# Optimization experiments

Measured on AMD Instinct MI355X. Metric: run time of the kernel, lower is better.

Reference implementation:

```python
import jax, jax.numpy as jnp
import numpy as np

DIM = 1024
NUM_HEADS = 16
HEAD_DIM = DIM // NUM_HEADS
SCALE = HEAD_DIM ** -0.25
EPS = 1e-5


def layer_norm(x, w, b):
    mu = jnp.mean(x, axis=-1, keepdims=True)
    var = jnp.var(x, axis=-1, keepdims=True)
    return (x - mu) * jax.lax.rsqrt(var + EPS) * w + b


def setup_inputs() -> dict:
    key = jax.random.key(0)
    ks = jax.random.split(key, 10)
    b, l, d = 2, 2048, DIM
    x = jax.random.normal(ks[0], (b, l, d), dtype=jnp.float32)
    # causal mask, broadcastable over heads: [b, 1, l, l]
    causal = jnp.tril(jnp.ones((l, l), dtype=jnp.int32))
    mask = jnp.broadcast_to(causal[None, None], (b, 1, l, l))
    s = 0.02
    return {
        "x": x,
        "mask": mask,
        "ln1_w": jnp.ones((d,), jnp.float32),
        "ln1_b": jnp.zeros((d,), jnp.float32),
        "qkv_w": jax.random.normal(ks[1], (d, 3 * d), jnp.float32) * s,
        "qkv_b": jnp.zeros((3 * d,), jnp.float32),
        "proj_w": jax.random.normal(ks[2], (d, d), jnp.float32) * s,
        "proj_b": jnp.zeros((d,), jnp.float32),
        "ln2_w": jnp.ones((d,), jnp.float32),
        "ln2_b": jnp.zeros((d,), jnp.float32),
        "ffn_w1": jax.random.normal(ks[3], (d, 4 * d), jnp.float32) * s,
        "ffn_b1": jnp.zeros((4 * d,), jnp.float32),
        "ffn_w2": jax.random.normal(ks[4], (4 * d, d), jnp.float32) * s,
        "ffn_b2": jnp.zeros((d,), jnp.float32),
    }


def attention(x, mask, qkv_w, qkv_b, proj_w, proj_b):
    b, l, d = x.shape
    n, c = NUM_HEADS, HEAD_DIM
    qkv = (x @ qkv_w + qkv_b).reshape(b, l, n * 3, c)
    q, k, v = qkv[:, :, :n], qkv[:, :, n:2 * n], qkv[:, :, 2 * n:]
    # scores: [b, n, l, l], scale applied to both q and k (head_dim^-0.25 each)
    attn = jnp.einsum('binc,bjnc->bnij', q * SCALE, k * SCALE)
    attn = jnp.where(mask[:, :, :l, :l] == 0, -jnp.inf, attn)
    attn = jax.nn.softmax(attn.astype(jnp.float32), axis=-1).astype(x.dtype)
    out = jnp.einsum('bnij,bjnc->binc', attn, v).reshape(b, l, d)
    return out @ proj_w + proj_b


def reference(x, mask, ln1_w, ln1_b, qkv_w, qkv_b, proj_w, proj_b,
              ln2_w, ln2_b, ffn_w1, ffn_b1, ffn_w2, ffn_b2):
    h = x + attention(layer_norm(x, ln1_w, ln1_b), mask, qkv_w, qkv_b, proj_w, proj_b)
    y = layer_norm(h, ln2_w, ln2_b)
    ffn = jax.nn.gelu(y @ ffn_w1 + ffn_b1, approximate=False) @ ffn_w2 + ffn_b2
    return h + ffn
```

## Files before the change

kernel.cpp:

```cpp
#include <hip/hip_runtime.h>
#include <hip/hip_bf16.h>
#include <math.h>

typedef __attribute__((ext_vector_type(8))) short bf16x8;
typedef __attribute__((ext_vector_type(4))) float f32x4;
typedef __attribute__((ext_vector_type(4))) unsigned u32x4;

#define MFMA16(a, b, c) __builtin_amdgcn_mfma_f32_16x16x32_bf16((a), (b), (c), 0, 0, 0)

typedef const __attribute__((address_space(1))) void* gas_ptr;
typedef __attribute__((address_space(3))) void* las_ptr;

#define QK_SCALE 0.18033688011112042f

__device__ __forceinline__ unsigned pack_bf16(float a, float b) {
    unsigned ua = (unsigned)__bfloat16_as_ushort(__float2bfloat16(a));
    unsigned ub = (unsigned)__bfloat16_as_ushort(__float2bfloat16(b));
    return ua | (ub << 16);
}

__global__ __launch_bounds__(256)
void transpose_all(const float* __restrict__ qkv_w, const float* __restrict__ proj_w,
                   const float* __restrict__ ffn_w1, const float* __restrict__ ffn_w2,
                   __hip_bfloat16* __restrict__ wqkv, __hip_bfloat16* __restrict__ wproj,
                   __hip_bfloat16* __restrict__ wff1, __hip_bfloat16* __restrict__ wff2)
{
    const int bid = blockIdx.x;
    const float* in; __hip_bfloat16* out; int K, N, r;
    if (bid < 3072)      { in = qkv_w;  out = wqkv;  K = 1024; N = 3072; r = bid;        }
    else if (bid < 4096) { in = proj_w; out = wproj; K = 1024; N = 1024; r = bid - 3072; }
    else if (bid < 8192) { in = ffn_w1; out = wff1;  K = 1024; N = 4096; r = bid - 4096; }
    else                 { in = ffn_w2; out = wff2;  K = 4096; N = 1024; r = bid - 8192; }
    const int ncols = N >> 5;
    const int n0 = (r % ncols) * 32, k0 = (r / ncols) * 32;

    __shared__ float t[32][33];
    const int tx = threadIdx.x & 31, ty = threadIdx.x >> 5;
    #pragma unroll
    for (int j = 0; j < 32; j += 8)
        t[ty + j][tx] = in[(size_t)(k0 + ty + j) * N + n0 + tx];
    __syncthreads();
    #pragma unroll
    for (int j = 0; j < 32; j += 8)
        out[(size_t)(n0 + ty + j) * K + k0 + tx] = __float2bfloat16(t[tx][ty + j]);
}

__global__ __launch_bounds__(256)
void ln_kernel(const float* __restrict__ in, const float* __restrict__ w,
               const float* __restrict__ b, __hip_bfloat16* __restrict__ out)
{
    const int row = blockIdx.x;
    const int tid = threadIdx.x;
    const float4 v = reinterpret_cast<const float4*>(in + (size_t)row * 1024)[tid];
    float s  = v.x + v.y + v.z + v.w;
    float s2 = v.x * v.x + v.y * v.y + v.z * v.z + v.w * v.w;
    #pragma unroll
    for (int off = 32; off > 0; off >>= 1) {
        s  += __shfl_down(s,  off);
        s2 += __shfl_down(s2, off);
    }
    __shared__ float red[8];
    const int wv = tid >> 6, ln = tid & 63;
    if (ln == 0) { red[wv] = s; red[4 + wv] = s2; }
    __syncthreads();
    s  = red[0] + red[1] + red[2] + red[3];
    s2 = red[4] + red[5] + red[6] + red[7];
    const float mu   = s * (1.0f / 1024.0f);
    const float var  = s2 * (1.0f / 1024.0f) - mu * mu;
    const float rstd = rsqrtf(var + 1e-5f);
    const float4 wv4 = reinterpret_cast<const float4*>(w)[tid];
    const float4 bv4 = reinterpret_cast<const float4*>(b)[tid];
    const size_t o = (size_t)row * 1024 + tid * 4;
    out[o + 0] = __float2bfloat16((v.x - mu) * rstd * wv4.x + bv4.x);
    out[o + 1] = __float2bfloat16((v.y - mu) * rstd * wv4.y + bv4.y);
    out[o + 2] = __float2bfloat16((v.z - mu) * rstd * wv4.z + bv4.z);
    out[o + 3] = __float2bfloat16((v.w - mu) * rstd * wv4.w + bv4.w);
}

template<int MODE>
__global__ __launch_bounds__(256, 3)
void gemm128p(const __hip_bfloat16* __restrict__ A,
              const __hip_bfloat16* __restrict__ Bt,
              const float* __restrict__ bias,
              void* __restrict__ C0, void* __restrict__ C1,
              int N, int K)
{
    constexpr int SLOT = 8192;
    __shared__ __align__(16) __hip_bfloat16 lds[3 * SLOT];

    const int tid  = threadIdx.x;
    const int lane = tid & 63;
    const int w    = tid >> 6;
    const int wr   = w >> 1, wc = w & 1;
    const int fr   = lane & 15, fq = lane >> 4;

    const int nwg = gridDim.x * gridDim.y;
    int flat = blockIdx.y * gridDim.x + blockIdx.x;
    flat = (flat & 7) * (nwg >> 3) + (flat >> 3);
    const int bx = flat % gridDim.x, by = flat / gridDim.x;
    const int m0 = by * 128, n0 = bx * 128;
    const int NT = K >> 5;

    const int prc = w * 8 + (lane >> 3);
    const int ch  = lane & 7;
    const __hip_bfloat16* aS[2];
    const __hip_bfloat16* bS[2];
    #pragma unroll
    for (int j = 0; j < 2; ++j) {
        const int pr  = prc + 32 * j;
        const int v   = ch ^ (pr & 7);
        const int row = 2 * pr + (v >> 2);
        const int col = 8 * (v & 3);
        aS[j] = A  + (size_t)(m0 + row) * K + col;
        bS[j] = Bt + (size_t)(n0 + row) * K + col;
    }

    auto stage = [&](int kt, int s) {
        __hip_bfloat16* LA = &lds[s * SLOT];
        __hip_bfloat16* LB = LA + 4096;
        #pragma unroll
        for (int j = 0; j < 2; ++j) {
            __builtin_amdgcn_global_load_lds((gas_ptr)(const void*)(aS[j] + kt * 32),
                                             (las_ptr)(void*)(LA + w * 512 + j * 2048), 16, 0, 0);
            __builtin_amdgcn_global_load_lds((gas_ptr)(const void*)(bS[j] + kt * 32),
                                             (las_ptr)(void*)(LB + w * 512 + j * 2048), 16, 0, 0);
        }
    };

    f32x4 acc[4][4] = {};

    stage(0, 0);
    stage(1, 1);
    int sl = 0, sp = 2;

    for (int kt = 0; kt < NT; ++kt) {
        if (kt + 1 < NT)
            asm volatile("s_waitcnt vmcnt(4) lgkmcnt(0)" ::: "memory");
        else
            asm volatile("s_waitcnt vmcnt(0) lgkmcnt(0)" ::: "memory");
        __builtin_amdgcn_s_barrier();
        __builtin_amdgcn_sched_barrier(0);

        if (kt + 2 < NT) stage(kt + 2, sp);

        const __hip_bfloat16* LA = &lds[sl * SLOT];
        const __hip_bfloat16* LB = LA + 4096;
        bf16x8 af[4], bg[4];
        #pragma unroll
        for (int m = 0; m < 4; ++m) {
            const int r = wr * 64 + m * 16 + fr;
            af[m] = *reinterpret_cast<const bf16x8*>(
                &LA[(r >> 1) * 64 + (((r & 1) * 32 + fq * 8) ^ (((r >> 1) & 7) * 8))]);
        }
        #pragma unroll
        for (int n = 0; n < 4; ++n) {
            const int r = wc * 64 + n * 16 + fr;
            bg[n] = *reinterpret_cast<const bf16x8*>(
                &LB[(r >> 1) * 64 + (((r & 1) * 32 + fq * 8) ^ (((r >> 1) & 7) * 8))]);
        }

        __builtin_amdgcn_s_setprio(1);
        #pragma unroll
        for (int m = 0; m < 4; ++m)
            #pragma unroll
            for (int n = 0; n < 4; ++n)
                acc[m][n] = MFMA16(af[m], bg[n], acc[m][n]);
        __builtin_amdgcn_s_setprio(0);

        sl = (sl == 2) ? 0 : sl + 1;
        sp = (sp == 2) ? 0 : sp + 1;
    }

    __syncthreads();
    ushort* E = reinterpret_cast<ushort*>(lds);
    auto eaddr = [](int r, int c16) { return r * 128 + (((c16) ^ ((r >> 3) & 15)) << 3); };

    const float qsc = (MODE == 3 && n0 < 1024) ? QK_SCALE : 1.0f;
    #pragma unroll
    for (int n = 0; n < 4; ++n) {
        const int col = wc * 64 + n * 16 + fr;
        const float bv = bias[n0 + col];
        #pragma unroll
        for (int m = 0; m < 4; ++m) {
            #pragma unroll
            for (int i = 0; i < 4; ++i) {
                const int row = wr * 64 + m * 16 + fq * 4 + i;
                float v = acc[m][n][i] + bv;
                if (MODE == 2) v = 0.5f * v * (1.0f + erff(v * 0.70710678118654752f));
                if (MODE == 3) v *= qsc;
                E[eaddr(row, col >> 3) + (col & 7)] =
                    __bfloat16_as_ushort(__float2bfloat16(v));
            }
        }
    }
    __syncthreads();

    if (MODE == 3 && n0 >= 2048) {
        const int bq    = m0 >> 11;
        const int lbase = m0 & 2047;
        const int hcb   = n0 - 2048;
        #pragma unroll
        for (int p = 0; p < 8; ++p) {
            const int id  = p * 256 + tid;
            const int hcl = id >> 4;
            const int lc  = id & 15;
            u32x4 pkt;
            #pragma unroll
            for (int k2 = 0; k2 < 4; ++k2) {
                const int l0 = lc * 8 + k2 * 2;
                const unsigned a = E[eaddr(l0,     hcl >> 3) + (hcl & 7)];
                const unsigned b = E[eaddr(l0 + 1, hcl >> 3) + (hcl & 7)];
                pkt[k2] = a | (b << 16);
            }
            *reinterpret_cast<u32x4*>(
                &reinterpret_cast<__hip_bfloat16*>(C1)
                    [((size_t)(bq * 1024 + hcb + hcl) << 11) + lbase + lc * 8]) = pkt;
        }
        return;
    }

    const size_t ldC = (MODE == 3) ? 2048 : (size_t)N;
    __hip_bfloat16* Cb = reinterpret_cast<__hip_bfloat16*>(C0);
    #pragma unroll
    for (int p = 0; p < 8; ++p) {
        const int id  = p * 256 + tid;
        const int row = id >> 4;
        const int c16 = id & 15;
        const bf16x8 vv = *reinterpret_cast<const bf16x8*>(&E[eaddr(row, c16)]);
        *reinterpret_cast<bf16x8*>(&Cb[(size_t)(m0 + row) * ldC + n0 + c16 * 8]) = vv;
    }
}

__global__ __launch_bounds__(512, 1)
void gemm256g(const __hip_bfloat16* __restrict__ A,
              const __hip_bfloat16* __restrict__ Bt,
              const float* __restrict__ bias,
              __hip_bfloat16* __restrict__ C0,
              int N, int K)
{
    constexpr int SLOT = 16384;
    __shared__ __align__(16) __hip_bfloat16 lds[4 * SLOT];

    const int tid  = threadIdx.x;
    const int lane = tid & 63;
    const int w    = tid >> 6;
    const int wm   = w >> 2, wn = w & 3;
    const int fr   = lane & 15, fq = lane >> 4;

    const int nwg = gridDim.x * gridDim.y;
    int flat = blockIdx.y * gridDim.x + blockIdx.x;
    flat = (flat & 7) * (nwg >> 3) + (flat >> 3);
    const int bx = flat % gridDim.x, by = flat / gridDim.x;
    const int m0 = by * 256, n0 = bx * 256;
    const int NT = K >> 5;

    const __hip_bfloat16* aS[2];
    const __hip_bfloat16* bS[2];
    #pragma unroll
    for (int j = 0; j < 2; ++j) {
        const int c   = tid + 512 * j;
        const int row = c >> 2;
        const int lc  = (c & 3) ^ ((row >> 1) & 3);
        aS[j] = A  + (size_t)(m0 + row) * K + lc * 8;
        bS[j] = Bt + (size_t)(n0 + row) * K + lc * 8;
    }

    auto stageA = [&](int kt) {
        __hip_bfloat16* L = &lds[(kt & 3) * SLOT];
        #pragma unroll
        for (int j = 0; j < 2; ++j)
            __builtin_amdgcn_global_load_lds((gas_ptr)(const void*)(aS[j] + kt * 32),
                                             (las_ptr)(void*)(L + w * 512 + j * 4096), 16, 0, 0);
    };
    auto stageB = [&](int kt) {
        __hip_bfloat16* L = &lds[(kt & 3) * SLOT] + 8192;
        #pragma unroll
        for (int j = 0; j < 2; ++j)
            __builtin_amdgcn_global_load_lds((gas_ptr)(const void*)(bS[j] + kt * 32),
                                             (las_ptr)(void*)(L + w * 512 + j * 4096), 16, 0, 0);
    };

    f32x4 acc[8][4] = {};

    stageA(0); stageB(0);
    stageA(1); stageB(1);
    stageA(2); stageB(2);
    asm volatile("s_waitcnt vmcnt(8)" ::: "memory");
    __builtin_amdgcn_s_barrier();
    __builtin_amdgcn_sched_barrier(0);

    for (int kt = 0; kt < NT; ++kt) {
        const __hip_bfloat16* LA = &lds[(kt & 3) * SLOT];
        const __hip_bfloat16* LB = LA + 8192;
        bf16x8 af[4], bg[4];

        #pragma unroll
        for (int m = 0; m < 4; ++m) {
            const int r = wm * 128 + m * 16 + fr;
            af[m] = *reinterpret_cast<const bf16x8*>(
                &LA[r * 32 + ((fq ^ ((r >> 1) & 3)) << 3)]);
        }
        #pragma unroll
        for (int n = 0; n < 4; ++n) {
            const int r = wn * 64 + n * 16 + fr;
            bg[n] = *reinterpret_cast<const bf16x8*>(
                &LB[r * 32 + ((fq ^ ((r >> 1) & 3)) << 3)]);
        }
        if (kt + 3 < NT) stageA(kt + 3);
        __builtin_amdgcn_sched_barrier(0);
        __builtin_amdgcn_s_barrier();
        asm volatile("s_waitcnt lgkmcnt(0)" ::: "memory");
        __builtin_amdgcn_sched_barrier(0);
        __builtin_amdgcn_s_setprio(1);
        #pragma unroll
        for (int m = 0; m < 4; ++m)
            #pragma unroll
            for (int n = 0; n < 4; ++n)
                acc[m][n] = MFMA16(af[m], bg[n], acc[m][n]);
        __builtin_amdgcn_s_setprio(0);
        __builtin_amdgcn_sched_barrier(0);
        __builtin_amdgcn_s_barrier();

        #pragma unroll
        for (int m = 0; m < 4; ++m) {
            const int r = wm * 128 + 64 + m * 16 + fr;
            af[m] = *reinterpret_cast<const bf16x8*>(
                &LA[r * 32 + ((fq ^ ((r >> 1) & 3)) << 3)]);
        }
        if (kt + 3 < NT) stageB(kt + 3);
        __builtin_amdgcn_sched_barrier(0);
        __builtin_amdgcn_s_barrier();
        asm volatile("s_waitcnt lgkmcnt(0)" ::: "memory");
        __builtin_amdgcn_sched_barrier(0);
        __builtin_amdgcn_s_setprio(1);
        #pragma unroll
        for (int m = 0; m < 4; ++m)
            #pragma unroll
            for (int n = 0; n < 4; ++n)
                acc[4 + m][n] = MFMA16(af[m], bg[n], acc[4 + m][n]);
        __builtin_amdgcn_s_setprio(0);
        __builtin_amdgcn_sched_barrier(0);
        if (kt + 3 < NT)      asm volatile("s_waitcnt vmcnt(8)" ::: "memory");
        else if (kt + 2 < NT) asm volatile("s_waitcnt vmcnt(4)" ::: "memory");
        else                  asm volatile("s_waitcnt vmcnt(0)" ::: "memory");
        __builtin_amdgcn_s_barrier();
    }

    __syncthreads();
    ushort* E = reinterpret_cast<ushort*>(lds);
    auto eaddr = [](int r, int c16) { return r * 256 + (((c16) ^ (r & 31)) << 3); };

    #pragma unroll
    for (int n = 0; n < 4; ++n) {
        const int col = wn * 64 + n * 16 + fr;
        const float bv = bias[n0 + col];
        #pragma unroll
        for (int a = 0; a < 8; ++a) {
            #pragma unroll
            for (int i = 0; i < 4; ++i) {
                const int row = wm * 128 + (a >> 2) * 64 + (a & 3) * 16 + fq * 4 + i;
                float v = acc[a][n][i] + bv;
                v = 0.5f * v * (1.0f + erff(v * 0.70710678118654752f));
                E[eaddr(row, col >> 3) + (col & 7)] =
                    __bfloat16_as_ushort(__float2bfloat16(v));
            }
        }
    }
    __syncthreads();

    #pragma unroll
    for (int p = 0; p < 16; ++p) {
        const int id  = p * 512 + tid;
        const int row = id >> 5;
        const int c16 = id & 31;
        const bf16x8 vv = *reinterpret_cast<const bf16x8*>(&E[eaddr(row, c16)]);
        *reinterpret_cast<bf16x8*>(&C0[(size_t)(m0 + row) * N + n0 + c16 * 8]) = vv;
    }
}

__global__ __launch_bounds__(256, 3)
void gemm_n64(const __hip_bfloat16* __restrict__ A,
              const __hip_bfloat16* __restrict__ Bt,
              const float* __restrict__ bias,
              const float* __restrict__ resid,
              float* __restrict__ C0,
              int N, int K)
{
    constexpr int SLOT = 6144;
    __shared__ __align__(16) __hip_bfloat16 lds[3 * SLOT];

    const int tid  = threadIdx.x;
    const int lane = tid & 63;
    const int w    = tid >> 6;
    const int wr   = w >> 1, wc = w & 1;
    const int fr   = lane & 15, fq = lane >> 4;

    const int nwg = gridDim.x * gridDim.y;
    int flat = blockIdx.y * gridDim.x + blockIdx.x;
    flat = (flat & 7) * (nwg >> 3) + (flat >> 3);
    const int bx = flat % gridDim.x, by = flat / gridDim.x;
    const int m0 = by * 128, n0 = bx * 64;
    const int NT = K >> 5;

    const int prc = w * 8 + (lane >> 3);
    const int ch  = lane & 7;
    const __hip_bfloat16* aS[2];
    #pragma unroll
    for (int j = 0; j < 2; ++j) {
        const int pr  = prc + 32 * j;
        const int v   = ch ^ (pr & 7);
        aS[j] = A + (size_t)(m0 + 2 * pr + (v >> 2)) * K + 8 * (v & 3);
    }
    const __hip_bfloat16* bS;
    {
        const int c  = w * 64 + lane;
        const int pr = c >> 3;
        const int v  = (c & 7) ^ (pr & 7);
        bS = Bt + (size_t)(n0 + 2 * pr + (v >> 2)) * K + 8 * (v & 3);
    }

    auto stage = [&](int kt, int s) {
        __hip_bfloat16* LA = &lds[s * SLOT];
        __hip_bfloat16* LB = LA + 4096;
        #pragma unroll
        for (int j = 0; j < 2; ++j)
            __builtin_amdgcn_global_load_lds((gas_ptr)(const void*)(aS[j] + kt * 32),
                                             (las_ptr)(void*)(LA + w * 512 + j * 2048), 16, 0, 0);
        __builtin_amdgcn_global_load_lds((gas_ptr)(const void*)(bS + kt * 32),
                                         (las_ptr)(void*)(LB + w * 512), 16, 0, 0);
    };

    f32x4 acc[4][2] = {};

    stage(0, 0);
    stage(1, 1);
    int sl = 0, sp = 2;

    for (int kt = 0; kt < NT; ++kt) {
        if (kt + 1 < NT)
            asm volatile("s_waitcnt vmcnt(3) lgkmcnt(0)" ::: "memory");
        else
            asm volatile("s_waitcnt vmcnt(0) lgkmcnt(0)" ::: "memory");
        __builtin_amdgcn_s_barrier();
        __builtin_amdgcn_sched_barrier(0);

        if (kt + 2 < NT) stage(kt + 2, sp);

        const __hip_bfloat16* LA = &lds[sl * SLOT];
        const __hip_bfloat16* LB = LA + 4096;
        bf16x8 af[4], bg[2];
        #pragma unroll
        for (int m = 0; m < 4; ++m) {
            const int r = wr * 64 + m * 16 + fr;
            af[m] = *reinterpret_cast<const bf16x8*>(
                &LA[(r >> 1) * 64 + (((r & 1) * 32 + fq * 8) ^ (((r >> 1) & 7) * 8))]);
        }
        #pragma unroll
        for (int n = 0; n < 2; ++n) {
            const int r = wc * 32 + n * 16 + fr;
            bg[n] = *reinterpret_cast<const bf16x8*>(
                &LB[(r >> 1) * 64 + (((r & 1) * 32 + fq * 8) ^ (((r >> 1) & 7) * 8))]);
        }

        __builtin_amdgcn_s_setprio(1);
        #pragma unroll
        for (int m = 0; m < 4; ++m)
            #pragma unroll
            for (int n = 0; n < 2; ++n)
                acc[m][n] = MFMA16(af[m], bg[n], acc[m][n]);
        __builtin_amdgcn_s_setprio(0);

        sl = (sl == 2) ? 0 : sl + 1;
        sp = (sp == 2) ? 0 : sp + 1;
    }

    #pragma unroll
    for (int n = 0; n < 2; ++n) {
        const int col = n0 + wc * 32 + n * 16 + fr;
        const float bv = bias[col];
        #pragma unroll
        for (int m = 0; m < 4; ++m)
            #pragma unroll
            for (int i = 0; i < 4; ++i) {
                const int row = m0 + wr * 64 + m * 16 + fq * 4 + i;
                C0[(size_t)row * N + col] = acc[m][n][i] + bv + resid[(size_t)row * N + col];
            }
    }
}

__global__ __launch_bounds__(256)
void attn_kernel(const __hip_bfloat16* __restrict__ qk,
                 const __hip_bfloat16* __restrict__ Vt,
                 __hip_bfloat16* __restrict__ out)
{
    const int bid  = blockIdx.x;
    const int xcd  = bid & 7;
    const int rank = bid >> 3;
    const int panel = xcd * 4 + (rank & 3);
    const int qt   = 31 - (rank >> 2);
    const int h = panel & 15, b = panel >> 4;
    const int q0 = qt * 64;

    const int lane = threadIdx.x & 63;
    const int w    = threadIdx.x >> 6;
    const int fr   = lane & 15, fq = lane >> 4;
    const int qrow = q0 + w * 16 + fr;

    __shared__ __align__(16) __hip_bfloat16 Klds[2][64 * 64];
    __shared__ __align__(16) __hip_bfloat16 Vlds[2][64 * 64];

    bf16x8 qf[2];
    {
        const __hip_bfloat16* qp = qk + ((size_t)(b * 2048 + qrow) << 11) + h * 64 + fq * 8;
        qf[0] = *reinterpret_cast<const bf16x8*>(qp);
        qf[1] = *reinterpret_cast<const bf16x8*>(qp + 32);
    }

    const int srow8 = lane >> 3;
    const int sc    = lane & 7;
    const __hip_bfloat16* Kg[2];
    const __hip_bfloat16* Vg[2];
    #pragma unroll
    for (int j = 0; j < 2; ++j) {
        const int r = w * 16 + j * 8 + srow8;
        const int csw = (sc ^ (r & 7)) * 8;
        Kg[j] = qk + ((size_t)(b * 2048 + r) << 11) + 1024 + h * 64 + csw;
        Vg[j] = Vt + ((size_t)(b * 1024 + h * 64 + r) << 11) + csw;
    }

    auto stage = [&](int kv0, int bufi) {
        __hip_bfloat16* KL = &Klds[bufi][0];
        __hip_bfloat16* VL = &Vlds[bufi][0];
        #pragma unroll
        for (int j = 0; j < 2; ++j) {
            __builtin_amdgcn_global_load_lds(
                (gas_ptr)(const void*)(Kg[j] + ((size_t)kv0 << 11)),
                (las_ptr)(void*)&KL[(w * 16 + j * 8) * 64], 16, 0, 0);
            __builtin_amdgcn_global_load_lds(
                (gas_ptr)(const void*)(Vg[j] + kv0),
                (las_ptr)(void*)&VL[(w * 16 + j * 8) * 64], 16, 0, 0);
        }
    };

    float m_run = -1e30f, l_run = 0.0f;
    f32x4 o[4] = {};

    const int ntiles = qt + 1;
    stage(0, 0);
    int cur = 0;

    for (int t = 0; t < ntiles; ++t) {
        const int kv0 = t << 6;
        __syncthreads();
        if (t + 1 < ntiles) stage((t + 1) << 6, cur ^ 1);

        const __hip_bfloat16* Kl = &Klds[cur][0];
        const __hip_bfloat16* Vl = &Vlds[cur][0];

        f32x4 s[4] = {};
        #pragma unroll
        for (int n = 0; n < 4; ++n) {
            const int row = n * 16 + fr;
            const int sw = (row & 7) << 3;
            const bf16x8 k0 = *reinterpret_cast<const bf16x8*>(&Kl[row * 64 + ((fq * 8) ^ sw)]);
            const bf16x8 k1 = *reinterpret_cast<const bf16x8*>(&Kl[row * 64 + ((fq * 8 + 32) ^ sw)]);
            s[n] = MFMA16(k0, qf[0], s[n]);
            s[n] = MFMA16(k1, qf[1], s[n]);
        }

        float pm = -1e30f;
        if (t == ntiles - 1) {
            #pragma unroll
            for (int n = 0; n < 4; ++n)
                #pragma unroll
                for (int i = 0; i < 4; ++i) {
                    const int kvp = kv0 + n * 16 + fq * 4 + i;
                    float sv = s[n][i];
                    sv = (kvp <= qrow) ? sv : -1e30f;
                    s[n][i] = sv;
                    pm = fmaxf(pm, sv);
                }
        } else {
            #pragma unroll
            for (int n = 0; n < 4; ++n)
                #pragma unroll
                for (int i = 0; i < 4; ++i)
                    pm = fmaxf(pm, s[n][i]);
        }
        pm = fmaxf(pm, __shfl_xor(pm, 16));
        pm = fmaxf(pm, __shfl_xor(pm, 32));

        if (!__all(pm <= m_run + 8.0f)) {
            const float mnew = fmaxf(m_run, pm);
            const float corr = exp2f(m_run - mnew);
            m_run = mnew;
            l_run *= corr;
            #pragma unroll
            for (int i = 0; i < 4; ++i) {
                const float ci = __shfl(corr, fq * 4 + i);
                o[0][i] *= ci; o[1][i] *= ci; o[2][i] *= ci; o[3][i] *= ci;
            }
        }

        float rs = 0.0f;
        unsigned pk[8];
        #pragma unroll
        for (int n = 0; n < 4; ++n) {
            const float p0 = exp2f(s[n][0] - m_run);
            const float p1 = exp2f(s[n][1] - m_run);
            const float p2 = exp2f(s[n][2] - m_run);
            const float p3 = exp2f(s[n][3] - m_run);
            rs += (p0 + p1) + (p2 + p3);
            pk[n * 2 + 0] = pack_bf16(p0, p1);
            pk[n * 2 + 1] = pack_bf16(p2, p3);
        }
        rs += __shfl_xor(rs, 16);
        rs += __shfl_xor(rs, 32);
        l_run += rs;

        u32x4 A0, A1;
        #pragma unroll
        for (int r = 0; r < 4; ++r) {
            const int slx = fr + ((2 * (fq & 1) + (r >> 1)) << 4);
            const unsigned lo0 = __shfl(pk[0 + (r & 1)], slx);
            const unsigned hi0 = __shfl(pk[2 + (r & 1)], slx);
            const unsigned lo1 = __shfl(pk[4 + (r & 1)], slx);
            const unsigned hi1 = __shfl(pk[6 + (r & 1)], slx);
            A0[r] = (fq & 2) ? hi0 : lo0;
            A1[r] = (fq & 2) ? hi1 : lo1;
        }
        const bf16x8 pa0 = __builtin_bit_cast(bf16x8, A0);
        const bf16x8 pa1 = __builtin_bit_cast(bf16x8, A1);

        #pragma unroll
        for (int tt = 0; tt < 4; ++tt) {
            const int row = tt * 16 + fr;
            const int sw = (row & 7) << 3;
            const bf16x8 v0 = *reinterpret_cast<const bf16x8*>(&Vl[row * 64 + ((fq * 8) ^ sw)]);
            const bf16x8 v1 = *reinterpret_cast<const bf16x8*>(&Vl[row * 64 + ((fq * 8 + 32) ^ sw)]);
            o[tt] = MFMA16(pa0, v0, o[tt]);
            o[tt] = MFMA16(pa1, v1, o[tt]);
        }
        cur ^= 1;
    }

    #pragma unroll
    for (int i = 0; i < 4; ++i) {
        const float li  = __shfl(l_run, fq * 4 + i);
        const float inv = 1.0f / li;
        const int row = q0 + w * 16 + fq * 4 + i;
        #pragma unroll
        for (int tt = 0; tt < 4; ++tt)
            out[(size_t)(b * 2048 + row) * 1024 + h * 64 + tt * 16 + fr] =
                __float2bfloat16(o[tt][i] * inv);
    }
}

extern "C" void kernel_launch(void* const* d_in, const int* in_sizes, int n_in,
                              void* d_out, int out_size, void* d_ws, size_t ws_size,
                              hipStream_t stream)
{
    (void)in_sizes; (void)n_in; (void)out_size; (void)ws_size;
    const float* x      = (const float*)d_in[0];
    const float* ln1_w  = (const float*)d_in[2];
    const float* ln1_b  = (const float*)d_in[3];
    const float* qkv_w  = (const float*)d_in[4];
    const float* qkv_b  = (const float*)d_in[5];
    const float* proj_w = (const float*)d_in[6];
    const float* proj_b = (const float*)d_in[7];
    const float* ln2_w  = (const float*)d_in[8];
    const float* ln2_b  = (const float*)d_in[9];
    const float* ffn_w1 = (const float*)d_in[10];
    const float* ffn_b1 = (const float*)d_in[11];
    const float* ffn_w2 = (const float*)d_in[12];
    const float* ffn_b2 = (const float*)d_in[13];
    float* outp = (float*)d_out;

    char* ws = (char*)d_ws;
    size_t off = 0;
    auto take = [&](size_t bytes) -> char* {
        char* p = ws + off;
        off += (bytes + 255) & ~(size_t)255;
        return p;
    };
    __hip_bfloat16* wqkv  = (__hip_bfloat16*)take((size_t)3072 * 1024 * 2);
    __hip_bfloat16* wproj = (__hip_bfloat16*)take((size_t)1024 * 1024 * 2);
    __hip_bfloat16* wff1  = (__hip_bfloat16*)take((size_t)4096 * 1024 * 2);
    __hip_bfloat16* wff2  = (__hip_bfloat16*)take((size_t)1024 * 4096 * 2);
    float*          hbuf  = (float*)take((size_t)4096 * 1024 * 4);
    __hip_bfloat16* xn    = (__hip_bfloat16*)take((size_t)4096 * 1024 * 2);
    __hip_bfloat16* qkb   = (__hip_bfloat16*)take((size_t)4096 * 2048 * 2);
    __hip_bfloat16* Vt    = (__hip_bfloat16*)take((size_t)2048 * 2048 * 2);
    __hip_bfloat16* attn  = (__hip_bfloat16*)take((size_t)4096 * 1024 * 2);
    __hip_bfloat16* ffn1  = qkb;

    transpose_all<<<12288, 256, 0, stream>>>(qkv_w, proj_w, ffn_w1, ffn_w2,
                                             wqkv, wproj, wff1, wff2);
    ln_kernel<<<4096, 256, 0, stream>>>(x, ln1_w, ln1_b, xn);
    gemm128p<3><<<dim3(24, 32), 256, 0, stream>>>(
        xn, wqkv, qkv_b, qkb, Vt, 3072, 1024);
    attn_kernel<<<1024, 256, 0, stream>>>(qkb, Vt, attn);
    gemm_n64<<<dim3(16, 32), 256, 0, stream>>>(
        attn, wproj, proj_b, x, hbuf, 1024, 1024);
    ln_kernel<<<4096, 256, 0, stream>>>(hbuf, ln2_w, ln2_b, xn);
    gemm256g<<<dim3(16, 16), 512, 0, stream>>>(
        xn, wff1, ffn_b1, ffn1, 4096, 1024);
    gemm_n64<<<dim3(16, 32), 256, 0, stream>>>(
        ffn1, wff2, ffn_b2, hbuf, outp, 1024, 4096);
}
```

Baseline: 244.2 us.

## Switch attention to 32x32 MFMA with two waves per block and staged output

```diff
diff --git a/kernel.cpp b/kernel.cpp
--- a/kernel.cpp
+++ b/kernel.cpp
@@ -4,9 +4,11 @@
 
 typedef __attribute__((ext_vector_type(8))) short bf16x8;
 typedef __attribute__((ext_vector_type(4))) float f32x4;
+typedef __attribute__((ext_vector_type(16))) float f32x16;
 typedef __attribute__((ext_vector_type(4))) unsigned u32x4;
 
 #define MFMA16(a, b, c) __builtin_amdgcn_mfma_f32_16x16x32_bf16((a), (b), (c), 0, 0, 0)
+#define MFMA32(a, b, c) __builtin_amdgcn_mfma_f32_32x32x16_bf16((a), (b), (c), 0, 0, 0)
 
 typedef const __attribute__((address_space(1))) void* gas_ptr;
 typedef __attribute__((address_space(3))) void* las_ptr;
@@ -488,7 +490,7 @@
     }
 }
 
-__global__ __launch_bounds__(256)
+__global__ __launch_bounds__(128)
 void attn_kernel(const __hip_bfloat16* __restrict__ qk,
                  const __hip_bfloat16* __restrict__ Vt,
                  __hip_bfloat16* __restrict__ out)
@@ -503,47 +505,46 @@
 
     const int lane = threadIdx.x & 63;
     const int w    = threadIdx.x >> 6;
-    const int fr   = lane & 15, fq = lane >> 4;
-    const int qrow = q0 + w * 16 + fr;
+    const int qv   = lane & 31;
+    const int hi   = lane >> 5;
+    const int qrow = q0 + w * 32 + qv;
 
     __shared__ __align__(16) __hip_bfloat16 Klds[2][64 * 64];
     __shared__ __align__(16) __hip_bfloat16 Vlds[2][64 * 64];
 
-    bf16x8 qf[2];
+    bf16x8 qf[4];
     {
-        const __hip_bfloat16* qp = qk + ((size_t)(b * 2048 + qrow) << 11) + h * 64 + fq * 8;
-        qf[0] = *reinterpret_cast<const bf16x8*>(qp);
-        qf[1] = *reinterpret_cast<const bf16x8*>(qp + 32);
-    }
-
-    const int srow8 = lane >> 3;
-    const int sc    = lane & 7;
-    const __hip_bfloat16* Kg[2];
-    const __hip_bfloat16* Vg[2];
-    #pragma unroll
-    for (int j = 0; j < 2; ++j) {
-        const int r = w * 16 + j * 8 + srow8;
-        const int csw = (sc ^ (r & 7)) * 8;
-        Kg[j] = qk + ((size_t)(b * 2048 + r) << 11) + 1024 + h * 64 + csw;
-        Vg[j] = Vt + ((size_t)(b * 1024 + h * 64 + r) << 11) + csw;
+        const __hip_bfloat16* qp = qk + ((size_t)(b * 2048 + qrow) << 11) + h * 64 + hi * 8;
+        #pragma unroll
+        for (int s = 0; s < 4; ++s)
+            qf[s] = *reinterpret_cast<const bf16x8*>(qp + s * 16);
+    }
+
+    const __hip_bfloat16* Kg[4];
+    const __hip_bfloat16* Vg[4];
+    #pragma unroll
+    for (int j = 0; j < 4; ++j) {
+        const int c  = w * 64 + j * 128 + lane;
+        const int r  = c >> 3;
+        const int lc = (c & 7) ^ (r & 7);
+        Kg[j] = qk + ((size_t)(b * 2048 + r) << 11) + 1024 + h * 64 + lc * 8;
+        Vg[j] = Vt + ((size_t)(b * 1024 + h * 64 + r) << 11) + lc * 8;
     }
 
     auto stage = [&](int kv0, int bufi) {
-        __hip_bfloat16* KL = &Klds[bufi][0];
-        __hip_bfloat16* VL = &Vlds[bufi][0];
-        #pragma unroll
-        for (int j = 0; j < 2; ++j) {
+        #pragma unroll
+        for (int j = 0; j < 4; ++j) {
             __builtin_amdgcn_global_load_lds(
                 (gas_ptr)(const void*)(Kg[j] + ((size_t)kv0 << 11)),
-                (las_ptr)(void*)&KL[(w * 16 + j * 8) * 64], 16, 0, 0);
+                (las_ptr)(void*)&Klds[bufi][(w * 64 + j * 128) * 8], 16, 0, 0);
             __builtin_amdgcn_global_load_lds(
                 (gas_ptr)(const void*)(Vg[j] + kv0),
-                (las_ptr)(void*)&VL[(w * 16 + j * 8) * 64], 16, 0, 0);
+                (las_ptr)(void*)&Vlds[bufi][(w * 64 + j * 128) * 8], 16, 0, 0);
         }
     };
 
     float m_run = -1e30f, l_run = 0.0f;
-    f32x4 o[4] = {};
+    f32x16 o0 = {}, o1 = {};
 
     const int ntiles = qt + 1;
     stage(0, 0);
@@ -557,37 +558,31 @@
         const __hip_bfloat16* Kl = &Klds[cur][0];
         const __hip_bfloat16* Vl = &Vlds[cur][0];
 
-        f32x4 s[4] = {};
-        #pragma unroll
-        for (int n = 0; n < 4; ++n) {
-            const int row = n * 16 + fr;
-            const int sw = (row & 7) << 3;
-            const bf16x8 k0 = *reinterpret_cast<const bf16x8*>(&Kl[row * 64 + ((fq * 8) ^ sw)]);
-            const bf16x8 k1 = *reinterpret_cast<const bf16x8*>(&Kl[row * 64 + ((fq * 8 + 32) ^ sw)]);
-            s[n] = MFMA16(k0, qf[0], s[n]);
-            s[n] = MFMA16(k1, qf[1], s[n]);
+        f32x16 s0 = {}, s1 = {};
+        #pragma unroll
+        for (int s = 0; s < 4; ++s) {
+            const int lc = 2 * s + hi;
+            const int ph = (lc ^ (qv & 7)) << 3;
+            const bf16x8 k0 = *reinterpret_cast<const bf16x8*>(&Kl[qv * 64 + ph]);
+            const bf16x8 k1 = *reinterpret_cast<const bf16x8*>(&Kl[(32 + qv) * 64 + ph]);
+            s0 = MFMA32(k0, qf[s], s0);
+            s1 = MFMA32(k1, qf[s], s1);
         }
 
         float pm = -1e30f;
         if (t == ntiles - 1) {
             #pragma unroll
-            for (int n = 0; n < 4; ++n)
-                #pragma unroll
-                for (int i = 0; i < 4; ++i) {
-                    const int kvp = kv0 + n * 16 + fq * 4 + i;
-                    float sv = s[n][i];
-                    sv = (kvp <= qrow) ? sv : -1e30f;
-                    s[n][i] = sv;
-                    pm = fmaxf(pm, sv);
-                }
+            for (int r = 0; r < 16; ++r) {
+                const int kvl = (r & 3) + 8 * (r >> 2) + 4 * hi;
+                s0[r] = (kv0 + kvl      <= qrow) ? s0[r] : -1e30f;
+                s1[r] = (kv0 + kvl + 32 <= qrow) ? s1[r] : -1e30f;
+                pm = fmaxf(pm, fmaxf(s0[r], s1[r]));
+            }
         } else {
             #pragma unroll
-            for (int n = 0; n < 4; ++n)
-                #pragma unroll
-                for (int i = 0; i < 4; ++i)
-                    pm = fmaxf(pm, s[n][i]);
-        }
-        pm = fmaxf(pm, __shfl_xor(pm, 16));
+            for (int r = 0; r < 16; ++r)
+                pm = fmaxf(pm, fmaxf(s0[r], s1[r]));
+        }
         pm = fmaxf(pm, __shfl_xor(pm, 32));
 
         if (!__all(pm <= m_run + 8.0f)) {
@@ -596,63 +591,66 @@
             m_run = mnew;
             l_run *= corr;
             #pragma unroll
-            for (int i = 0; i < 4; ++i) {
-                const float ci = __shfl(corr, fq * 4 + i);
-                o[0][i] *= ci; o[1][i] *= ci; o[2][i] *= ci; o[3][i] *= ci;
-            }
+            for (int r = 0; r < 16; ++r) { o0[r] *= corr; o1[r] *= corr; }
         }
 
         float rs = 0.0f;
-        unsigned pk[8];
-        #pragma unroll
-        for (int n = 0; n < 4; ++n) {
-            const float p0 = exp2f(s[n][0] - m_run);
-            const float p1 = exp2f(s[n][1] - m_run);
-            const float p2 = exp2f(s[n][2] - m_run);
-            const float p3 = exp2f(s[n][3] - m_run);
-            rs += (p0 + p1) + (p2 + p3);
-            pk[n * 2 + 0] = pack_bf16(p0, p1);
-            pk[n * 2 + 1] = pack_bf16(p2, p3);
-        }
-        rs += __shfl_xor(rs, 16);
+        unsigned pk0[8], pk1[8];
+        #pragma unroll
+        for (int j = 0; j < 8; ++j) {
+            const float a0 = exp2f(s0[2 * j]     - m_run);
+            const float a1 = exp2f(s0[2 * j + 1] - m_run);
+            const float b0 = exp2f(s1[2 * j]     - m_run);
+            const float b1 = exp2f(s1[2 * j + 1] - m_run);
+            rs += (a0 + a1) + (b0 + b1);
+            pk0[j] = pack_bf16(a0, a1);
+            pk1[j] = pack_bf16(b0, b1);
+        }
         rs += __shfl_xor(rs, 32);
         l_run += rs;
 
-        u32x4 A0, A1;
-        #pragma unroll
-        for (int r = 0; r < 4; ++r) {
-            const int slx = fr + ((2 * (fq & 1) + (r >> 1)) << 4);
-            const unsigned lo0 = __shfl(pk[0 + (r & 1)], slx);
-            const unsigned hi0 = __shfl(pk[2 + (r & 1)], slx);
-            const unsigned lo1 = __shfl(pk[4 + (r & 1)], slx);
-            const unsigned hi1 = __shfl(pk[6 + (r & 1)], slx);
-            A0[r] = (fq & 2) ? hi0 : lo0;
-            A1[r] = (fq & 2) ? hi1 : lo1;
-        }
-        const bf16x8 pa0 = __builtin_bit_cast(bf16x8, A0);
-        const bf16x8 pa1 = __builtin_bit_cast(bf16x8, A1);
-
-        #pragma unroll
-        for (int tt = 0; tt < 4; ++tt) {
-            const int row = tt * 16 + fr;
-            const int sw = (row & 7) << 3;
-            const bf16x8 v0 = *reinterpret_cast<const bf16x8*>(&Vl[row * 64 + ((fq * 8) ^ sw)]);
-            const bf16x8 v1 = *reinterpret_cast<const bf16x8*>(&Vl[row * 64 + ((fq * 8 + 32) ^ sw)]);
-            o[tt] = MFMA16(pa0, v0, o[tt]);
-            o[tt] = MFMA16(pa1, v1, o[tt]);
+        #pragma unroll
+        for (int s = 0; s < 4; ++s) {
+            const int s2 = (s & 1) * 4;
+            unsigned e0, e1, e2, e3;
+            if (s < 2) { e0 = pk0[s2]; e1 = pk0[s2 + 1]; e2 = pk0[s2 + 2]; e3 = pk0[s2 + 3]; }
+            else       { e0 = pk1[s2]; e1 = pk1[s2 + 1]; e2 = pk1[s2 + 2]; e3 = pk1[s2 + 3]; }
+            asm("v_permlane32_swap_b32 %0, %1" : "+v"(e0), "+v"(e2));
+            asm("v_permlane32_swap_b32 %0, %1" : "+v"(e1), "+v"(e3));
+            u32x4 B; B[0] = e0; B[1] = e1; B[2] = e2; B[3] = e3;
+            const bf16x8 pb = __builtin_bit_cast(bf16x8, B);
+
+            const int lc = 2 * s + hi;
+            const int ph = (lc ^ (qv & 7)) << 3;
+            const bf16x8 v0 = *reinterpret_cast<const bf16x8*>(&Vl[qv * 64 + ph]);
+            const bf16x8 v1 = *reinterpret_cast<const bf16x8*>(&Vl[(32 + qv) * 64 + ph]);
+            o0 = MFMA32(v0, pb, o0);
+            o1 = MFMA32(v1, pb, o1);
         }
         cur ^= 1;
     }
 
-    #pragma unroll
-    for (int i = 0; i < 4; ++i) {
-        const float li  = __shfl(l_run, fq * 4 + i);
-        const float inv = 1.0f / li;
-        const int row = q0 + w * 16 + fq * 4 + i;
-        #pragma unroll
-        for (int tt = 0; tt < 4; ++tt)
-            out[(size_t)(b * 2048 + row) * 1024 + h * 64 + tt * 16 + fr] =
-                __float2bfloat16(o[tt][i] * inv);
+    const float inv = 1.0f / l_run;
+    __syncthreads();
+    ushort* OS = reinterpret_cast<ushort*>(&Klds[0][0]);
+    const int orow = w * 32 + qv;
+    #pragma unroll
+    for (int j = 0; j < 8; ++j) {
+        const int d = 2 * (j & 1) + 8 * (j >> 1) + 4 * hi;
+        *reinterpret_cast<unsigned*>(&OS[orow * 72 + d]) =
+            pack_bf16(o0[2 * j] * inv, o0[2 * j + 1] * inv);
+        *reinterpret_cast<unsigned*>(&OS[orow * 72 + d + 32]) =
+            pack_bf16(o1[2 * j] * inv, o1[2 * j + 1] * inv);
+    }
+    __syncthreads();
+    #pragma unroll
+    for (int p = 0; p < 4; ++p) {
+        const int c   = p * 128 + threadIdx.x;
+        const int row = c >> 3;
+        const int ch  = c & 7;
+        const bf16x8 vv = *reinterpret_cast<const bf16x8*>(&OS[row * 72 + ch * 8]);
+        *reinterpret_cast<bf16x8*>(
+            &out[(size_t)(b * 2048 + q0 + row) * 1024 + h * 64 + ch * 8]) = vv;
     }
 }
 
@@ -699,7 +697,7 @@
     ln_kernel<<<4096, 256, 0, stream>>>(x, ln1_w, ln1_b, xn);
     gemm128p<3><<<dim3(24, 32), 256, 0, stream>>>(
         xn, wqkv, qkv_b, qkb, Vt, 3072, 1024);
-    attn_kernel<<<1024, 256, 0, stream>>>(qkb, Vt, attn);
+    attn_kernel<<<1024, 128, 0, stream>>>(qkb, Vt, attn);
     gemm_n64<<<dim3(16, 32), 256, 0, stream>>>(
         attn, wproj, proj_b, x, hbuf, 1024, 1024);
     ln_kernel<<<4096, 256, 0, stream>>>(hbuf, ln2_w, ln2_b, xn);
```

After: 253.2 us. 3.7% more time.

## Process two 64-row query tiles per attention block to reuse K/V loads

Applied to the files above, without the earlier changes.

```diff
diff --git a/kernel.cpp b/kernel.cpp
--- a/kernel.cpp
+++ b/kernel.cpp
@@ -497,23 +497,28 @@
     const int xcd  = bid & 7;
     const int rank = bid >> 3;
     const int panel = xcd * 4 + (rank & 3);
-    const int qt   = 31 - (rank >> 2);
+    const int r4   = rank >> 2;
+    const int qt   = (r4 < 8) ? (15 - 2 * r4) : (2 * (r4 - 8));
     const int h = panel & 15, b = panel >> 4;
-    const int q0 = qt * 64;
+    const int q0 = qt * 128;
 
     const int lane = threadIdx.x & 63;
     const int w    = threadIdx.x >> 6;
     const int fr   = lane & 15, fq = lane >> 4;
-    const int qrow = q0 + w * 16 + fr;
+    const int qrowA = q0 + w * 16 + fr;
+    const int qrowB = qrowA + 64;
 
     __shared__ __align__(16) __hip_bfloat16 Klds[2][64 * 64];
     __shared__ __align__(16) __hip_bfloat16 Vlds[2][64 * 64];
 
-    bf16x8 qf[2];
+    bf16x8 qfA[2], qfB[2];
     {
-        const __hip_bfloat16* qp = qk + ((size_t)(b * 2048 + qrow) << 11) + h * 64 + fq * 8;
-        qf[0] = *reinterpret_cast<const bf16x8*>(qp);
-        qf[1] = *reinterpret_cast<const bf16x8*>(qp + 32);
+        const __hip_bfloat16* qpA = qk + ((size_t)(b * 2048 + qrowA) << 11) + h * 64 + fq * 8;
+        qfA[0] = *reinterpret_cast<const bf16x8*>(qpA);
+        qfA[1] = *reinterpret_cast<const bf16x8*>(qpA + 32);
+        const __hip_bfloat16* qpB = qk + ((size_t)(b * 2048 + qrowB) << 11) + h * 64 + fq * 8;
+        qfB[0] = *reinterpret_cast<const bf16x8*>(qpB);
+        qfB[1] = *reinterpret_cast<const bf16x8*>(qpB + 32);
     }
 
     const int srow8 = lane >> 3;
@@ -542,10 +547,10 @@
         }
     };
 
-    float m_run = -1e30f, l_run = 0.0f;
-    f32x4 o[4] = {};
-
-    const int ntiles = qt + 1;
+    float mA = -1e30f, lA = 0.0f, mB = -1e30f, lB = 0.0f;
+    f32x4 oA[4] = {}, oB[4] = {};
+
+    const int ntiles = 2 * qt + 2;
     stage(0, 0);
     int cur = 0;
 
@@ -557,102 +562,191 @@
         const __hip_bfloat16* Kl = &Klds[cur][0];
         const __hip_bfloat16* Vl = &Vlds[cur][0];
 
-        f32x4 s[4] = {};
+        bf16x8 kf0[4], kf1[4];
         #pragma unroll
         for (int n = 0; n < 4; ++n) {
             const int row = n * 16 + fr;
             const int sw = (row & 7) << 3;
-            const bf16x8 k0 = *reinterpret_cast<const bf16x8*>(&Kl[row * 64 + ((fq * 8) ^ sw)]);
-            const bf16x8 k1 = *reinterpret_cast<const bf16x8*>(&Kl[row * 64 + ((fq * 8 + 32) ^ sw)]);
-            s[n] = MFMA16(k0, qf[0], s[n]);
-            s[n] = MFMA16(k1, qf[1], s[n]);
-        }
-
-        float pm = -1e30f;
-        if (t == ntiles - 1) {
-            #pragma unroll
-            for (int n = 0; n < 4; ++n)
-                #pragma unroll
-                for (int i = 0; i < 4; ++i) {
-                    const int kvp = kv0 + n * 16 + fq * 4 + i;
-                    float sv = s[n][i];
-                    sv = (kvp <= qrow) ? sv : -1e30f;
-                    s[n][i] = sv;
-                    pm = fmaxf(pm, sv);
-                }
-        } else {
-            #pragma unroll
-            for (int n = 0; n < 4; ++n)
-                #pragma unroll
-                for (int i = 0; i < 4; ++i)
-                    pm = fmaxf(pm, s[n][i]);
-        }
-        pm = fmaxf(pm, __shfl_xor(pm, 16));
-        pm = fmaxf(pm, __shfl_xor(pm, 32));
-
-        if (!__all(pm <= m_run + 8.0f)) {
-            const float mnew = fmaxf(m_run, pm);
-            const float corr = exp2f(m_run - mnew);
-            m_run = mnew;
-            l_run *= corr;
-            #pragma unroll
-            for (int i = 0; i < 4; ++i) {
-                const float ci = __shfl(corr, fq * 4 + i);
-                o[0][i] *= ci; o[1][i] *= ci; o[2][i] *= ci; o[3][i] *= ci;
-            }
-        }
-
-        float rs = 0.0f;
-        unsigned pk[8];
+            kf0[n] = *reinterpret_cast<const bf16x8*>(&Kl[row * 64 + ((fq * 8) ^ sw)]);
+            kf1[n] = *reinterpret_cast<const bf16x8*>(&Kl[row * 64 + ((fq * 8 + 32) ^ sw)]);
+        }
+        f32x4 sA[4] = {}, sB[4] = {};
         #pragma unroll
         for (int n = 0; n < 4; ++n) {
-            const float p0 = exp2f(s[n][0] - m_run);
-            const float p1 = exp2f(s[n][1] - m_run);
-            const float p2 = exp2f(s[n][2] - m_run);
-            const float p3 = exp2f(s[n][3] - m_run);
-            rs += (p0 + p1) + (p2 + p3);
-            pk[n * 2 + 0] = pack_bf16(p0, p1);
-            pk[n * 2 + 1] = pack_bf16(p2, p3);
-        }
-        rs += __shfl_xor(rs, 16);
-        rs += __shfl_xor(rs, 32);
-        l_run += rs;
-
-        u32x4 A0, A1;
-        #pragma unroll
-        for (int r = 0; r < 4; ++r) {
-            const int slx = fr + ((2 * (fq & 1) + (r >> 1)) << 4);
-            const unsigned lo0 = __shfl(pk[0 + (r & 1)], slx);
-            const unsigned hi0 = __shfl(pk[2 + (r & 1)], slx);
-            const unsigned lo1 = __shfl(pk[4 + (r & 1)], slx);
-            const unsigned hi1 = __shfl(pk[6 + (r & 1)], slx);
-            A0[r] = (fq & 2) ? hi0 : lo0;
-            A1[r] = (fq & 2) ? hi1 : lo1;
-        }
-        const bf16x8 pa0 = __builtin_bit_cast(bf16x8, A0);
-        const bf16x8 pa1 = __builtin_bit_cast(bf16x8, A1);
-
+            sA[n] = MFMA16(kf0[n], qfA[0], sA[n]);
+            sA[n] = MFMA16(kf1[n], qfA[1], sA[n]);
+        }
+        #pragma unroll
+        for (int n = 0; n < 4; ++n) {
+            sB[n] = MFMA16(kf0[n], qfB[0], sB[n]);
+            sB[n] = MFMA16(kf1[n], qfB[1], sB[n]);
+        }
+
+        bf16x8 vf0[4], vf1[4];
         #pragma unroll
         for (int tt = 0; tt < 4; ++tt) {
             const int row = tt * 16 + fr;
             const int sw = (row & 7) << 3;
-            const bf16x8 v0 = *reinterpret_cast<const bf16x8*>(&Vl[row * 64 + ((fq * 8) ^ sw)]);
-            const bf16x8 v1 = *reinterpret_cast<const bf16x8*>(&Vl[row * 64 + ((fq * 8 + 32) ^ sw)]);
-            o[tt] = MFMA16(pa0, v0, o[tt]);
-            o[tt] = MFMA16(pa1, v1, o[tt]);
+            vf0[tt] = *reinterpret_cast<const bf16x8*>(&Vl[row * 64 + ((fq * 8) ^ sw)]);
+            vf1[tt] = *reinterpret_cast<const bf16x8*>(&Vl[row * 64 + ((fq * 8 + 32) ^ sw)]);
+        }
+
+        {
+            float pm = -1e30f;
+            if (t >= ntiles - 2) {
+                #pragma unroll
+                for (int n = 0; n < 4; ++n)
+                    #pragma unroll
+                    for (int i = 0; i < 4; ++i) {
+                        const int kvp = kv0 + n * 16 + fq * 4 + i;
+                        float sv = sA[n][i];
+                        sv = (kvp <= qrowA) ? sv : -1e30f;
+                        sA[n][i] = sv;
+                        pm = fmaxf(pm, sv);
+                    }
+            } else {
+                #pragma unroll
+                for (int n = 0; n < 4; ++n)
+                    #pragma unroll
+                    for (int i = 0; i < 4; ++i)
+                        pm = fmaxf(pm, sA[n][i]);
+            }
+            pm = fmaxf(pm, __shfl_xor(pm, 16));
+            pm = fmaxf(pm, __shfl_xor(pm, 32));
+            if (!__all(pm <= mA + 8.0f)) {
+                const float mnew = fmaxf(mA, pm);
+                const float corr = exp2f(mA - mnew);
+                mA = mnew;
+                lA *= corr;
+                #pragma unroll
+                for (int i = 0; i < 4; ++i) {
+                    const float ci = __shfl(corr, fq * 4 + i);
+                    oA[0][i] *= ci; oA[1][i] *= ci; oA[2][i] *= ci; oA[3][i] *= ci;
+                }
+            }
+            float rs = 0.0f;
+            unsigned pk[8];
+            #pragma unroll
+            for (int n = 0; n < 4; ++n) {
+                const float p0 = exp2f(sA[n][0] - mA);
+                const float p1 = exp2f(sA[n][1] - mA);
+                const float p2 = exp2f(sA[n][2] - mA);
+                const float p3 = exp2f(sA[n][3] - mA);
+                rs += (p0 + p1) + (p2 + p3);
+                pk[n * 2 + 0] = pack_bf16(p0, p1);
+                pk[n * 2 + 1] = pack_bf16(p2, p3);
+            }
+            rs += __shfl_xor(rs, 16);
+            rs += __shfl_xor(rs, 32);
+            lA += rs;
+
+            u32x4 A0, A1;
+            #pragma unroll
+            for (int r = 0; r < 4; ++r) {
+                const int slx = fr + ((2 * (fq & 1) + (r >> 1)) << 4);
+                const unsigned lo0 = __shfl(pk[0 + (r & 1)], slx);
+                const unsigned hi0 = __shfl(pk[2 + (r & 1)], slx);
+                const unsigned lo1 = __shfl(pk[4 + (r & 1)], slx);
+                const unsigned hi1 = __shfl(pk[6 + (r & 1)], slx);
+                A0[r] = (fq & 2) ? hi0 : lo0;
+                A1[r] = (fq & 2) ? hi1 : lo1;
+            }
+            const bf16x8 pa0 = __builtin_bit_cast(bf16x8, A0);
+            const bf16x8 pa1 = __builtin_bit_cast(bf16x8, A1);
+            #pragma unroll
+            for (int tt = 0; tt < 4; ++tt) {
+                oA[tt] = MFMA16(pa0, vf0[tt], oA[tt]);
+                oA[tt] = MFMA16(pa1, vf1[tt], oA[tt]);
+            }
+        }
+
+        {
+            float pm = -1e30f;
+            if (t == ntiles - 1) {
+                #pragma unroll
+                for (int n = 0; n < 4; ++n)
+                    #pragma unroll
+                    for (int i = 0; i < 4; ++i) {
+                        const int kvp = kv0 + n * 16 + fq * 4 + i;
+                        float sv = sB[n][i];
+                        sv = (kvp <= qrowB) ? sv : -1e30f;
+                        sB[n][i] = sv;
+                        pm = fmaxf(pm, sv);
+                    }
+            } else {
+                #pragma unroll
+                for (int n = 0; n < 4; ++n)
+                    #pragma unroll
+                    for (int i = 0; i < 4; ++i)
+                        pm = fmaxf(pm, sB[n][i]);
+            }
+            pm = fmaxf(pm, __shfl_xor(pm, 16));
+            pm = fmaxf(pm, __shfl_xor(pm, 32));
+            if (!__all(pm <= mB + 8.0f)) {
+                const float mnew = fmaxf(mB, pm);
+                const float corr = exp2f(mB - mnew);
+                mB = mnew;
+                lB *= corr;
+                #pragma unroll
+                for (int i = 0; i < 4; ++i) {
+                    const float ci = __shfl(corr, fq * 4 + i);
+                    oB[0][i] *= ci; oB[1][i] *= ci; oB[2][i] *= ci; oB[3][i] *= ci;
+                }
+            }
+            float rs = 0.0f;
+            unsigned pk[8];
+            #pragma unroll
+            for (int n = 0; n < 4; ++n) {
+                const float p0 = exp2f(sB[n][0] - mB);
+                const float p1 = exp2f(sB[n][1] - mB);
+                const float p2 = exp2f(sB[n][2] - mB);
+                const float p3 = exp2f(sB[n][3] - mB);
+                rs += (p0 + p1) + (p2 + p3);
+                pk[n * 2 + 0] = pack_bf16(p0, p1);
+                pk[n * 2 + 1] = pack_bf16(p2, p3);
+            }
+            rs += __shfl_xor(rs, 16);
+            rs += __shfl_xor(rs, 32);
+            lB += rs;
+
+            u32x4 A0, A1;
+            #pragma unroll
+            for (int r = 0; r < 4; ++r) {
+                const int slx = fr + ((2 * (fq & 1) + (r >> 1)) << 4);
+                const unsigned lo0 = __shfl(pk[0 + (r & 1)], slx);
+                const unsigned hi0 = __shfl(pk[2 + (r & 1)], slx);
+                const unsigned lo1 = __shfl(pk[4 + (r & 1)], slx);
+                const unsigned hi1 = __shfl(pk[6 + (r & 1)], slx);
+                A0[r] = (fq & 2) ? hi0 : lo0;
+                A1[r] = (fq & 2) ? hi1 : lo1;
+            }
+            const bf16x8 pa0 = __builtin_bit_cast(bf16x8, A0);
+            const bf16x8 pa1 = __builtin_bit_cast(bf16x8, A1);
+            #pragma unroll
+            for (int tt = 0; tt < 4; ++tt) {
+                oB[tt] = MFMA16(pa0, vf0[tt], oB[tt]);
+                oB[tt] = MFMA16(pa1, vf1[tt], oB[tt]);
+            }
         }
         cur ^= 1;
     }
 
     #pragma unroll
     for (int i = 0; i < 4; ++i) {
-        const float li  = __shfl(l_run, fq * 4 + i);
-        const float inv = 1.0f / li;
-        const int row = q0 + w * 16 + fq * 4 + i;
+        const float liA = __shfl(lA, fq * 4 + i);
+        const float invA = 1.0f / liA;
+        const int rowA = q0 + w * 16 + fq * 4 + i;
         #pragma unroll
         for (int tt = 0; tt < 4; ++tt)
-            out[(size_t)(b * 2048 + row) * 1024 + h * 64 + tt * 16 + fr] =
-                __float2bfloat16(o[tt][i] * inv);
+            out[(size_t)(b * 2048 + rowA) * 1024 + h * 64 + tt * 16 + fr] =
+                __float2bfloat16(oA[tt][i] * invA);
+        const float liB = __shfl(lB, fq * 4 + i);
+        const float invB = 1.0f / liB;
+        const int rowB = rowA + 64;
+        #pragma unroll
+        for (int tt = 0; tt < 4; ++tt)
+            out[(size_t)(b * 2048 + rowB) * 1024 + h * 64 + tt * 16 + fr] =
+                __float2bfloat16(oB[tt][i] * invB);
     }
 }
 
@@ -699,7 +793,7 @@
     ln_kernel<<<4096, 256, 0, stream>>>(x, ln1_w, ln1_b, xn);
     gemm128p<3><<<dim3(24, 32), 256, 0, stream>>>(
         xn, wqkv, qkv_b, qkb, Vt, 3072, 1024);
-    attn_kernel<<<1024, 256, 0, stream>>>(qkb, Vt, attn);
+    attn_kernel<<<512, 256, 0, stream>>>(qkb, Vt, attn);
     gemm_n64<<<dim3(16, 32), 256, 0, stream>>>(
         attn, wproj, proj_b, x, hbuf, 1024, 1024);
     ln_kernel<<<4096, 256, 0, stream>>>(hbuf, ln2_w, ln2_b, xn);
```

Result: slower. 261.4 us (+7.0%).
